# Optimization experiments

Hardware: AMD Instinct MI355X
Metric: run time of the kernel (lower is better)

The kernel has to match this reference:

```python
import jax, jax.numpy as jnp
import numpy as np

COMMITMENT_COST = 0.25

def setup_inputs() -> dict:
    key = jax.random.key(0)
    k1, k2 = jax.random.split(key)
    z = jax.random.normal(k1, (32768, 512), dtype=jnp.float32)
    # codebook initialized uniform(-1/K, 1/K) as in the torch module
    K = 8192
    W = jax.random.uniform(k2, (K, 512), dtype=jnp.float32, minval=-1.0 / K, maxval=1.0 / K)
    return {"z": z, "W": W}

def reference(z, W):
    # z: [B, D], W: [K, D]
    # squared-distance expansion: ||z||^2 + ||w||^2 - 2 z.w
    d2 = (jnp.sum(z * z, axis=1, keepdims=True)
          + jnp.sum(W * W, axis=1)
          - 2.0 * jnp.einsum('bd,kd->bk', z, W))  # [B, K]
    indices = jnp.argmin(d2, axis=1)              # [B]
    z_q_raw = W[indices]                          # [B, D]
    e_latent_loss = jnp.mean((jax.lax.stop_gradient(z_q_raw) - z) ** 2)
    q_latent_loss = jnp.mean((z_q_raw - jax.lax.stop_gradient(z)) ** 2)
    vq_loss = q_latent_loss + COMMITMENT_COST * e_latent_loss
    # straight-through estimator
    z_q = z + jax.lax.stop_gradient(z_q_raw - z)
    return (z_q, indices, vq_loss)
```

## Files before the change

### kernel.cpp

```cpp
#include <hip/hip_runtime.h>
#include <stdint.h>


#define B_ROWS 32768
#define DIM    512
#define KCODES 8192
#define SUPERS 4
#define TILES  16
#define ZROWS  64

typedef short bhalf8_t __attribute__((ext_vector_type(8)));
typedef float f32x4_t  __attribute__((ext_vector_type(4)));

__device__ __forceinline__ float b2f(unsigned short u) {
    return __uint_as_float(((unsigned int)u) << 16);
}
__device__ __forceinline__ unsigned short f2b(float f) {
    unsigned int x = __float_as_uint(f);
    return (unsigned short)((x + 0x7FFFu + ((x >> 16) & 1u)) >> 16);
}
__device__ __forceinline__ void gl_lds16(const void* g, void* l) {
    __builtin_amdgcn_global_load_lds(
        (const __attribute__((address_space(1))) unsigned int*)g,
        (__attribute__((address_space(3))) unsigned int*)l, 16, 0, 0);
}

__global__ __launch_bounds__(256) void k_split(const float4* __restrict__ src,
                                               ushort4* __restrict__ dst, int n4) {
    int i = blockIdx.x * 256 + threadIdx.x;
    int stride = gridDim.x * 256;
    for (; i < n4; i += stride) {
        float4 v = src[i];
        ushort4 h;
        h.x = f2b(v.x); h.y = f2b(v.y); h.z = f2b(v.z); h.w = f2b(v.w);
        dst[i] = h;
    }
}

__global__ __launch_bounds__(256) void k_pairsq(const float* __restrict__ X,
                                                float* __restrict__ out, int nrows) {
    int wid = threadIdx.x >> 6, lane = threadIdx.x & 63;
    int r = blockIdx.x * 4 + wid;
    if (r >= nrows) return;
    int b = lane >> 3, j = lane & 7;
    float acc = 0.f;
    if (b < 4) {
        const float* x = X + (size_t)r * DIM + b * 128 + j;
        float v = x[0];
        acc = __fmul_rn(v, v);
        for (int i = 1; i < 16; i++) {
            float w = x[8 * i];
            acc = __fadd_rn(acc, __fmul_rn(w, w));
        }
    }
    float t = __fadd_rn(acc, __shfl_xor(acc, 1));
    t = __fadd_rn(t, __shfl_xor(t, 2));
    t = __fadd_rn(t, __shfl_xor(t, 4));
    float u = __fadd_rn(t, __shfl_xor(t, 8));
    u = __fadd_rn(u, __shfl_xor(u, 16));
    if (lane == 0) out[r] = u;
}

__device__ __forceinline__ void compute_slice2(const unsigned char* zl, int ks,
                                               const unsigned char* wbuf,
                                               int wm, int wn, int lane,
                                               f32x4_t acc[2][4]) {
    bhalf8_t af[2], bf[4];
#pragma unroll
    for (int f = 0; f < 2; f++)
        af[f] = *(const bhalf8_t*)(zl + ks * 4096 + (wm * 2 + f) * 1024 + lane * 16);
#pragma unroll
    for (int f = 0; f < 4; f++)
        bf[f] = *(const bhalf8_t*)(wbuf + wn * 4096 + f * 1024 + lane * 16);
#pragma unroll
    for (int fm = 0; fm < 2; fm++)
#pragma unroll
        for (int fn = 0; fn < 4; fn++)
            acc[fm][fn] = __builtin_amdgcn_mfma_f32_16x16x32_bf16(af[fm], bf[fn], acc[fm][fn], 0, 0, 0);
}

__global__ __launch_bounds__(256) void k_argmin(const unsigned short* __restrict__ Zh,
                                                const unsigned short* __restrict__ Wh,
                                                const float* __restrict__ ww,
                                                float2* __restrict__ part) {
    __shared__ alignas(16) unsigned char smem[81920];
    const int tid = threadIdx.x;
    const int lane = tid & 63, w = tid >> 6;
    const int wm = w >> 1, wn = w & 1;
    const int lane15 = lane & 15, q = lane >> 4;
    const int b = blockIdx.x;
    const int super = b & 3;
    const int rb = (b >> 2) * ZROWS;

    unsigned char* zl  = smem;
    unsigned char* wl0 = smem + 65536;
    unsigned char* wl1 = smem + 65536 + 8192;

    {
        const int m = tid & 15;
        const int kseg8 = ((tid >> 4) & 3) << 3;
#pragma unroll
        for (int i = 0; i < 16; i++) {
            const int s = i * 256 + tid;
            const int ks = s >> 8;
            const int g = (s >> 6) & 3;
            gl_lds16(Zh + (size_t)(rb + g * 16 + m) * DIM + ks * 32 + kseg8,
                     zl + s * 16);
        }
    }

    const int rowO0 = ((tid >> 6) << 4) | (tid & 15);
    const int kO0   = ((tid >> 4) & 3) << 3;
    const int dst0  = tid * 16;

#define STAGE_W(ST, WB)                                                          \
    do {                                                                         \
        const int _tl = (ST) >> 4;                                               \
        const int _nt = super * 2048 + _tl * 128;                                \
        const int _kg = ((ST) & 15) * 32 + kO0;                                  \
        gl_lds16(Wh + (size_t)(_nt + rowO0) * DIM + _kg,      (WB) + dst0);      \
        gl_lds16(Wh + (size_t)(_nt + rowO0 + 64) * DIM + _kg, (WB) + 4096 + dst0);\
    } while (0)

    uint32_t p1[2][4], p2[2][4];
#pragma unroll
    for (int i = 0; i < 2; i++)
#pragma unroll
        for (int jj = 0; jj < 4; jj++) { p1[i][jj] = 0xFFFFFFFFu; p2[i][jj] = 0xFFFFFFFFu; }

    STAGE_W(0, wl0);
    __syncthreads();

    for (int tl = 0; tl < TILES; ++tl) {
        const int nt = super * 2048 + tl * 128;

        float cb[4];
#pragma unroll
        for (int fn = 0; fn < 4; fn++)
            cb[fn] = ww[nt + wn * 64 + fn * 16 + lane15] + 0.5f;

        f32x4_t acc[2][4];
#pragma unroll
        for (int i = 0; i < 2; i++)
#pragma unroll
            for (int jj = 0; jj < 4; jj++) acc[i][jj] = (f32x4_t){0.f, 0.f, 0.f, 0.f};

        for (int k2 = 0; k2 < 16; k2 += 2) {
            const int st = tl * 16 + k2;
            STAGE_W(st + 1, wl1);
            compute_slice2(zl, k2, wl0, wm, wn, lane, acc);
            __syncthreads();
            if (st + 2 < SUPERS * 0 + TILES * 16) {
                STAGE_W(st + 2, wl0);
            }
            compute_slice2(zl, k2 + 1, wl1, wm, wn, lane, acc);
            __syncthreads();
        }

#pragma unroll
        for (int fm = 0; fm < 2; fm++)
#pragma unroll
            for (int r = 0; r < 4; r++)
#pragma unroll
                for (int fn = 0; fn < 4; fn++) {
                    float sv = fmaf(-2.0f, acc[fm][fn][r], cb[fn]);
                    uint32_t pk = (__float_as_uint(sv) & 0xFFFFFF80u) | (uint32_t)(tl * 4 + fn);
                    if (pk < p1[fm][r]) { p2[fm][r] = p1[fm][r]; p1[fm][r] = pk; }
                    else if (pk < p2[fm][r]) { p2[fm][r] = pk; }
                }
    }
#undef STAGE_W

    __syncthreads();
    uint32_t* keys = (uint32_t*)smem;
#pragma unroll
    for (int fm = 0; fm < 2; fm++)
#pragma unroll
        for (int r = 0; r < 4; r++) {
            int row = wm * 32 + fm * 16 + q * 4 + r;
            int slice = wn * 16 + lane15;
            keys[row * 65 + slice * 2 + 0] = p1[fm][r];
            keys[row * 65 + slice * 2 + 1] = p2[fm][r];
        }
    __syncthreads();
    if (tid < ZROWS) {
        int row = tid;
        int rglob = rb + row;
        for (int s = 0; s < 4; s++) {
            uint32_t bk = 0xFFFFFFFFu; int be = 0;
            for (int e = 0; e < 64; e++) {
                uint32_t k = keys[row * 65 + e];
                if (k < bk) { bk = k; be = e; }
            }
            int slice = be >> 1;
            int id = (int)(bk & 127u);
            int n = super * 2048 + (id >> 2) * 128 + (slice >> 4) * 64 + (id & 3) * 16 + (slice & 15);
            part[((size_t)rglob * SUPERS + super) * 4 + s] =
                make_float2(__uint_as_float(bk), __int_as_float(n));
            keys[row * 65 + be] = 0xFFFFFFFFu;
        }
    }
}

__global__ __launch_bounds__(256) void k_exact(const float* __restrict__ Zf,
                                               const float* __restrict__ Wf,
                                               const float2* __restrict__ part,
                                               const float* __restrict__ zz,
                                               const float* __restrict__ ww,
                                               float* __restrict__ outf,
                                               float* __restrict__ lossp) {
    __shared__ float wsum[4];
    int wid = threadIdx.x >> 6, lane = threadIdx.x & 63;
    int r = blockIdx.x * 4 + wid;
    int c = lane >> 2, j = lane & 3;

    float2 P = part[((size_t)r * SUPERS + (c >> 2)) * 4 + (c & 3)];
    int n = __float_as_int(P.y);
    n = min(max(n, 0), KCODES - 1);

    const float* zp = Zf + (size_t)r * DIM + j;
    const float* wp = Wf + (size_t)n * DIM + j;
    float acc = 0.f;
    for (int i = 0; i < 128; i++)
        acc = __fadd_rn(acc, __fmul_rn(zp[4 * i], wp[4 * i]));
    float t = __fadd_rn(acc, __shfl_xor(acc, 1));
    t = __fadd_rn(t, __shfl_xor(t, 2));
    float dot = __shfl(t, c * 4);

    float t1 = __fadd_rn(zz[r], ww[n]);
    float t2 = __fmul_rn(2.0f, dot);
    float d2 = __fadd_rn(t1, -t2);

    float bd = (j == 0) ? d2 : 3.4e38f;
    int   bn = (j == 0) ? n  : 0x7FFFFFFF;
#pragma unroll
    for (int off = 32; off; off >>= 1) {
        float od = __shfl_xor(bd, off);
        int   on = __shfl_xor(bn, off);
        if (od < bd || (od == bd && on < bn)) { bd = od; bn = on; }
    }
    int idx = bn;

    float4 wa = *(const float4*)(Wf + (size_t)idx * DIM + lane * 8);
    float4 wb = *(const float4*)(Wf + (size_t)idx * DIM + lane * 8 + 4);
    float4 za = *(const float4*)(Zf + (size_t)r   * DIM + lane * 8);
    float4 zb = *(const float4*)(Zf + (size_t)r   * DIM + lane * 8 + 4);
    *(float4*)(outf + (size_t)r * DIM + lane * 8)     = wa;
    *(float4*)(outf + (size_t)r * DIM + lane * 8 + 4) = wb;
    float d0 = za.x - wa.x, d1 = za.y - wa.y, dd2 = za.z - wa.z, d3 = za.w - wa.w;
    float d4 = zb.x - wb.x, d5 = zb.y - wb.y, d6 = zb.z - wb.z, d7 = zb.w - wb.w;
    float ls = d0*d0 + d1*d1 + dd2*dd2 + d3*d3 + d4*d4 + d5*d5 + d6*d6 + d7*d7;
#pragma unroll
    for (int off = 32; off; off >>= 1) ls += __shfl_xor(ls, off);
    if (lane == 0) {
        outf[(size_t)B_ROWS * DIM + r] = (float)idx;
        wsum[wid] = ls;
    }
    __syncthreads();
    if (threadIdx.x == 0) lossp[blockIdx.x] = wsum[0] + wsum[1] + wsum[2] + wsum[3];
}

__global__ __launch_bounds__(256) void k_loss(const float* __restrict__ lossp,
                                              float* __restrict__ outf) {
    __shared__ float sm[256];
    float a = 0.f;
    for (int i = threadIdx.x; i < 8192; i += 256) a += lossp[i];
    sm[threadIdx.x] = a;
    __syncthreads();
    for (int s = 128; s; s >>= 1) {
        if (threadIdx.x < s) sm[threadIdx.x] += sm[threadIdx.x + s];
        __syncthreads();
    }
    if (threadIdx.x == 0)
        outf[(size_t)B_ROWS * DIM + B_ROWS] = 1.25f * sm[0] / 16777216.0f;
}

extern "C" void kernel_launch(void* const* d_in, const int* in_sizes, int n_in,
                              void* d_out, int out_size, void* d_ws, size_t ws_size,
                              hipStream_t stream) {
    (void)in_sizes; (void)n_in; (void)out_size; (void)ws_size;
    const float* Zf = (const float*)d_in[0];
    const float* Wf = (const float*)d_in[1];
    float* outf = (float*)d_out;

    unsigned short* Zh = (unsigned short*)d_out;
    unsigned short* Wh = (unsigned short*)((char*)d_out + (32ull << 20));

    float*  ww    = (float*)d_ws;
    float*  zz    = (float*)((char*)d_ws + 32768);
    float*  lossp = (float*)((char*)d_ws + 163840);
    float2* partp = (float2*)((char*)d_ws + 196608);

    k_split<<<1024, 256, 0, stream>>>((const float4*)Zf, (ushort4*)Zh, B_ROWS * DIM / 4);
    k_split<<<512,  256, 0, stream>>>((const float4*)Wf, (ushort4*)Wh, KCODES * DIM / 4);
    k_pairsq<<<KCODES / 4, 256, 0, stream>>>(Wf, ww, KCODES);
    k_pairsq<<<B_ROWS / 4, 256, 0, stream>>>(Zf, zz, B_ROWS);
    k_argmin<<<(B_ROWS / ZROWS) * SUPERS, 256, 0, stream>>>(Zh, Wh, ww, partp);
    k_exact<<<B_ROWS / 4, 256, 0, stream>>>(Zf, Wf, partp, zz, ww, outf, lossp);
    k_loss<<<1, 256, 0, stream>>>(lossp, outf);
}
```

Measured before the change: 844.9 us.

## Double waves per argmin block, splitting codebook columns across four waves

Launches the argmin kernel with 512 threads (8 waves) in place of 256. Each wave now computes a 32x32 sub-tile, not 32x64, so per-wave register use and MFMA work are halved, and W staging needs one load per thread. The aim is more waves in flight to hide LDS and global latency. In exchange, the per-row candidate merge now scans 128 keys, and the keys buffer (64 rows x 130 words) fits within the existing 80 KB of shared memory.

```diff
diff --git a/kernel.cpp b/kernel.cpp
--- a/kernel.cpp
+++ b/kernel.cpp
@@ -8,6 +8,7 @@
 #define SUPERS 4
 #define TILES  16
 #define ZROWS  64
+#define NSTEP  256
 
 typedef short bhalf8_t __attribute__((ext_vector_type(8)));
 typedef float f32x4_t  __attribute__((ext_vector_type(4)));
@@ -61,32 +62,32 @@
     if (lane == 0) out[r] = u;
 }
 
-__device__ __forceinline__ void compute_slice2(const unsigned char* zl, int ks,
-                                               const unsigned char* wbuf,
-                                               int wm, int wn, int lane,
-                                               f32x4_t acc[2][4]) {
-    bhalf8_t af[2], bf[4];
+__device__ __forceinline__ void compute_ks(const unsigned char* zl, int ks,
+                                           const unsigned char* wbuf,
+                                           int wm, int wn, int lane,
+                                           f32x4_t acc[2][2]) {
+    bhalf8_t af[2], bf[2];
 #pragma unroll
     for (int f = 0; f < 2; f++)
         af[f] = *(const bhalf8_t*)(zl + ks * 4096 + (wm * 2 + f) * 1024 + lane * 16);
 #pragma unroll
-    for (int f = 0; f < 4; f++)
-        bf[f] = *(const bhalf8_t*)(wbuf + wn * 4096 + f * 1024 + lane * 16);
+    for (int f = 0; f < 2; f++)
+        bf[f] = *(const bhalf8_t*)(wbuf + (wn * 2 + f) * 1024 + lane * 16);
 #pragma unroll
     for (int fm = 0; fm < 2; fm++)
 #pragma unroll
-        for (int fn = 0; fn < 4; fn++)
+        for (int fn = 0; fn < 2; fn++)
             acc[fm][fn] = __builtin_amdgcn_mfma_f32_16x16x32_bf16(af[fm], bf[fn], acc[fm][fn], 0, 0, 0);
 }
 
-__global__ __launch_bounds__(256) void k_argmin(const unsigned short* __restrict__ Zh,
+__global__ __launch_bounds__(512) void k_argmin(const unsigned short* __restrict__ Zh,
                                                 const unsigned short* __restrict__ Wh,
                                                 const float* __restrict__ ww,
                                                 float2* __restrict__ part) {
     __shared__ alignas(16) unsigned char smem[81920];
     const int tid = threadIdx.x;
     const int lane = tid & 63, w = tid >> 6;
-    const int wm = w >> 1, wn = w & 1;
+    const int wm = w >> 2, wn = w & 3;
     const int lane15 = lane & 15, q = lane >> 4;
     const int b = blockIdx.x;
     const int super = b & 3;
@@ -100,8 +101,8 @@
         const int m = tid & 15;
         const int kseg8 = ((tid >> 4) & 3) << 3;
 #pragma unroll
-        for (int i = 0; i < 16; i++) {
-            const int s = i * 256 + tid;
+        for (int i = 0; i < 8; i++) {
+            const int s = i * 512 + tid;
             const int ks = s >> 8;
             const int g = (s >> 6) & 3;
             gl_lds16(Zh + (size_t)(rb + g * 16 + m) * DIM + ks * 32 + kseg8,
@@ -109,17 +110,14 @@
         }
     }
 
-    const int rowO0 = ((tid >> 6) << 4) | (tid & 15);
-    const int kO0   = ((tid >> 4) & 3) << 3;
-    const int dst0  = tid * 16;
-
-#define STAGE_W(ST, WB)                                                          \
-    do {                                                                         \
-        const int _tl = (ST) >> 4;                                               \
-        const int _nt = super * 2048 + _tl * 128;                                \
-        const int _kg = ((ST) & 15) * 32 + kO0;                                  \
-        gl_lds16(Wh + (size_t)(_nt + rowO0) * DIM + _kg,      (WB) + dst0);      \
-        gl_lds16(Wh + (size_t)(_nt + rowO0 + 64) * DIM + _kg, (WB) + 4096 + dst0);\
+    const int colO = ((tid >> 6) << 4) | (tid & 15);
+    const int kO   = ((tid >> 4) & 3) << 3;
+    const int dst0 = tid * 16;
+#define STAGE_W(ST, WB)                                                     \
+    do {                                                                    \
+        const int _nt = super * 2048 + ((ST) >> 4) * 128;                   \
+        const int _kg = ((ST) & 15) * 32 + kO;                              \
+        gl_lds16(Wh + (size_t)(_nt + colO) * DIM + _kg, (WB) + dst0);       \
     } while (0)
 
     uint32_t p1[2][4], p2[2][4];
@@ -133,27 +131,22 @@
 
     for (int tl = 0; tl < TILES; ++tl) {
         const int nt = super * 2048 + tl * 128;
-
-        float cb[4];
-#pragma unroll
-        for (int fn = 0; fn < 4; fn++)
-            cb[fn] = ww[nt + wn * 64 + fn * 16 + lane15] + 0.5f;
-
-        f32x4_t acc[2][4];
+        float cb0 = ww[nt + wn * 32 + lane15] + 0.5f;
+        float cb1 = ww[nt + wn * 32 + 16 + lane15] + 0.5f;
+
+        f32x4_t acc[2][2];
 #pragma unroll
         for (int i = 0; i < 2; i++)
 #pragma unroll
-            for (int jj = 0; jj < 4; jj++) acc[i][jj] = (f32x4_t){0.f, 0.f, 0.f, 0.f};
+            for (int jj = 0; jj < 2; jj++) acc[i][jj] = (f32x4_t){0.f, 0.f, 0.f, 0.f};
 
         for (int k2 = 0; k2 < 16; k2 += 2) {
             const int st = tl * 16 + k2;
             STAGE_W(st + 1, wl1);
-            compute_slice2(zl, k2, wl0, wm, wn, lane, acc);
+            compute_ks(zl, k2, wl0, wm, wn, lane, acc);
             __syncthreads();
-            if (st + 2 < SUPERS * 0 + TILES * 16) {
-                STAGE_W(st + 2, wl0);
-            }
-            compute_slice2(zl, k2 + 1, wl1, wm, wn, lane, acc);
+            if (st + 2 < NSTEP) STAGE_W(st + 2, wl0);
+            compute_ks(zl, k2 + 1, wl1, wm, wn, lane, acc);
             __syncthreads();
         }
 
@@ -162,9 +155,9 @@
 #pragma unroll
             for (int r = 0; r < 4; r++)
 #pragma unroll
-                for (int fn = 0; fn < 4; fn++) {
-                    float sv = fmaf(-2.0f, acc[fm][fn][r], cb[fn]);
-                    uint32_t pk = (__float_as_uint(sv) & 0xFFFFFF80u) | (uint32_t)(tl * 4 + fn);
+                for (int fn = 0; fn < 2; fn++) {
+                    float sv = fmaf(-2.0f, acc[fm][fn][r], fn ? cb1 : cb0);
+                    uint32_t pk = (__float_as_uint(sv) & 0xFFFFFF80u) | (uint32_t)(tl * 2 + fn);
                     if (pk < p1[fm][r]) { p2[fm][r] = p1[fm][r]; p1[fm][r] = pk; }
                     else if (pk < p2[fm][r]) { p2[fm][r] = pk; }
                 }
@@ -178,9 +171,9 @@
 #pragma unroll
         for (int r = 0; r < 4; r++) {
             int row = wm * 32 + fm * 16 + q * 4 + r;
-            int slice = wn * 16 + lane15;
-            keys[row * 65 + slice * 2 + 0] = p1[fm][r];
-            keys[row * 65 + slice * 2 + 1] = p2[fm][r];
+            int sp = wn * 16 + lane15;
+            keys[row * 130 + sp * 2 + 0] = p1[fm][r];
+            keys[row * 130 + sp * 2 + 1] = p2[fm][r];
         }
     __syncthreads();
     if (tid < ZROWS) {
@@ -188,16 +181,16 @@
         int rglob = rb + row;
         for (int s = 0; s < 4; s++) {
             uint32_t bk = 0xFFFFFFFFu; int be = 0;
-            for (int e = 0; e < 64; e++) {
-                uint32_t k = keys[row * 65 + e];
+            for (int e = 0; e < 128; e++) {
+                uint32_t k = keys[row * 130 + e];
                 if (k < bk) { bk = k; be = e; }
             }
-            int slice = be >> 1;
+            int sp = be >> 1;
             int id = (int)(bk & 127u);
-            int n = super * 2048 + (id >> 2) * 128 + (slice >> 4) * 64 + (id & 3) * 16 + (slice & 15);
+            int n = super * 2048 + (id >> 1) * 128 + (sp >> 4) * 32 + (id & 1) * 16 + (sp & 15);
             part[((size_t)rglob * SUPERS + super) * 4 + s] =
                 make_float2(__uint_as_float(bk), __int_as_float(n));
-            keys[row * 65 + be] = 0xFFFFFFFFu;
+            keys[row * 130 + be] = 0xFFFFFFFFu;
         }
     }
 }
@@ -295,7 +288,7 @@
     k_split<<<512,  256, 0, stream>>>((const float4*)Wf, (ushort4*)Wh, KCODES * DIM / 4);
     k_pairsq<<<KCODES / 4, 256, 0, stream>>>(Wf, ww, KCODES);
     k_pairsq<<<B_ROWS / 4, 256, 0, stream>>>(Zf, zz, B_ROWS);
-    k_argmin<<<(B_ROWS / ZROWS) * SUPERS, 256, 0, stream>>>(Zh, Wh, ww, partp);
+    k_argmin<<<(B_ROWS / ZROWS) * SUPERS, 512, 0, stream>>>(Zh, Wh, ww, partp);
     k_exact<<<B_ROWS / 4, 256, 0, stream>>>(Zf, Wf, partp, zz, ww, outf, lossp);
     k_loss<<<1, 256, 0, stream>>>(lossp, outf);
 }
```

Measured after the change: 844.4 us. Within noise of the previous version (-0.0%).
